# Kernel tuning notes

Hardware: AMD Instinct MI355X
Metric: run time of the kernel (lower is better)

## Reference

```python
import jax, jax.numpy as jnp
import numpy as np

BIT = 4
TOPK = 4
COEFF = 0.01
THD_POS = 2 ** (BIT - 1) - 1   # symmetric: +7
THD_NEG = -THD_POS             # symmetric: -7  -> 15 levels


def setup_inputs() -> dict:
    key = jax.random.key(0)
    k1, k2 = jax.random.split(key)
    weight = jax.random.normal(k1, (4096, 4096), dtype=jnp.float32)
    # positive per-channel quant step sizes, shape [out, 1]
    scale = jax.random.uniform(k2, (4096, 1), dtype=jnp.float32, minval=0.005, maxval=0.05)
    return {"weight": weight, "scale": scale}


def reference(weight, scale):
    # quantization level indices: [-7 .. 7], 15 levels
    q_range = jnp.arange(THD_NEG, THD_POS + 1, dtype=jnp.float32)      # [L]
    centers = scale * q_range                                          # [O, L] (per-channel)
    # broadcast squared distances: [O, I, L]
    d2 = (weight[:, :, None] - centers[:, None, :]) ** 2
    # torch.topk defaults to largest=True -> take k LARGEST squared distances
    vals, _ = jax.lax.top_k(d2, TOPK)                                  # [O, I, K], descending
    sm = jax.nn.softmax(vals, axis=-1)                                 # [O, I, K]
    loss = jnp.sum(vals * (1.0 - sm)) / (TOPK - 1)
    return loss * COEFF
```

## Files before the change

kernel.cpp:

```cpp
#include <hip/hip_runtime.h>


#define BLOCK 256
#define GRID  4096
#define S_F4  (GRID * BLOCK)
#define TILES 4

__device__ __forceinline__ float elem_loss(float wv, float s7, float s6,
                                           float s5, float s4) {
    const float a  = fabsf(wv);
    const float L0 = a + s7, L1 = a + s6, L2 = a + s5, L3 = a + s4;
    const float r0 = fabsf(s7 - a), r1 = fabsf(s6 - a);
    const float t0 = fmaxf(L0, r0);
    const float t1 = __builtin_amdgcn_fmed3f(r0, L0, L1);
    const float t2 = __builtin_amdgcn_fmed3f(r0, L1, L2);
    const float t3 = __builtin_amdgcn_fmed3f(r0, L2, L3);
    const float u0 = fmaxf(t0, r1);
    const float u1 = __builtin_amdgcn_fmed3f(r1, t0, t1);
    const float u2 = __builtin_amdgcn_fmed3f(r1, t1, t2);
    const float u3 = __builtin_amdgcn_fmed3f(r1, t2, t3);
    const float v0 = u0*u0, v1 = u1*u1, v2 = u2*u2, v3 = u3*u3;
    const float e1 = __expf(v1 - v0);
    const float e2 = __expf(v2 - v0);
    const float e3 = __expf(v3 - v0);
    const float Z   = 1.f + e1 + e2 + e3;
    const float dot = fmaf(v3, e3, fmaf(v2, e2, fmaf(v1, e1, v0)));
    return ((v0 + v1) + (v2 + v3)) - __fdividef(dot, Z);
}

__device__ __forceinline__ float quad_loss(float4 w4, float s) {
    const float s7 = 7.f*s, s6 = 6.f*s, s5 = 5.f*s, s4 = 4.f*s;
    return (elem_loss(w4.x, s7, s6, s5, s4) + elem_loss(w4.y, s7, s6, s5, s4))
         + (elem_loss(w4.z, s7, s6, s5, s4) + elem_loss(w4.w, s7, s6, s5, s4));
}

__global__ __launch_bounds__(BLOCK) void partial_kernel(
    const float4* __restrict__ w,
    const float* __restrict__ scale,
    float* __restrict__ partial)
{
    const int tid   = blockIdx.x * BLOCK + threadIdx.x;
    const int rbase = tid >> 10;

    float4 cw = w[tid];
    float  cs = scale[rbase];

    float acc = 0.f;
    #pragma unroll
    for (int m = 0; m < TILES; ++m) {
        float4 nw; float ns;
        if (m + 1 < TILES) {
            nw = w[tid + (m + 1) * S_F4];
            ns = scale[rbase + (m + 1) * 1024];
        }
        acc += quad_loss(cw, cs);
        if (m + 1 < TILES) { cw = nw; cs = ns; }
    }

    #pragma unroll
    for (int off = 32; off > 0; off >>= 1)
        acc += __shfl_down(acc, off, 64);
    __shared__ float lds[BLOCK / 64];
    const int lane = threadIdx.x & 63, wid = threadIdx.x >> 6;
    if (lane == 0) lds[wid] = acc;
    __syncthreads();
    if (threadIdx.x == 0) {
        float t = 0.f;
        #pragma unroll
        for (int q = 0; q < BLOCK / 64; ++q) t += lds[q];
        partial[blockIdx.x] = t;
    }
}

__global__ __launch_bounds__(1024) void reduce_kernel(
    const float* __restrict__ partial, float* __restrict__ out)
{
    float v = 0.f;
    #pragma unroll
    for (int k = 0; k < GRID / 1024; ++k)
        v += partial[threadIdx.x + k * 1024];
    #pragma unroll
    for (int off = 32; off > 0; off >>= 1)
        v += __shfl_down(v, off, 64);
    __shared__ float lds[16];
    const int lane = threadIdx.x & 63, wid = threadIdx.x >> 6;
    if (lane == 0) lds[wid] = v;
    __syncthreads();
    if (threadIdx.x == 0) {
        float t = 0.f;
        #pragma unroll
        for (int q = 0; q < 16; ++q) t += lds[q];
        out[0] = t * (0.01f / 3.0f);
    }
}

extern "C" void kernel_launch(void* const* d_in, const int* in_sizes, int n_in,
                              void* d_out, int out_size, void* d_ws, size_t ws_size,
                              hipStream_t stream) {
    const float4* weight4 = (const float4*)d_in[0];
    const float*  scale   = (const float*)d_in[1];
    float* out     = (float*)d_out;
    float* partial = (float*)d_ws;
    partial_kernel<<<GRID, BLOCK, 0, stream>>>(weight4, scale, partial);
    reduce_kernel<<<1, 1024, 0, stream>>>(partial, out);
}
```

Measured before the change: 104.0 us.

## Fold log2e into inputs, simplify top-k network, prefetch two tiles ahead

Scales weights and steps by sqrt(log2 e) so the softmax uses raw exp2 directly, and multiplies the final sum by ln2 to undo the scaling. Uses the fact that the largest distance is always |w|+7s to drop one max/med3 stage, and replaces the fast divide with rcp plus fma. Also deepens the load prefetch to two tiles ahead and adds an occupancy hint to launch bounds. The aim is fewer VALU instructions per element and better hiding of memory latency, at the cost of more registers and slightly different rounding.

```diff
diff --git a/kernel.cpp b/kernel.cpp
--- a/kernel.cpp
+++ b/kernel.cpp
@@ -5,36 +5,39 @@
 #define GRID  4096
 #define S_F4  (GRID * BLOCK)
 #define TILES 4
+#define C_SQRT_LOG2E 1.2011224087864498f
+#define LN2 0.69314718055994531f
 
 __device__ __forceinline__ float elem_loss(float wv, float s7, float s6,
                                            float s5, float s4) {
-    const float a  = fabsf(wv);
+    const float a  = fabsf(wv) * C_SQRT_LOG2E;
     const float L0 = a + s7, L1 = a + s6, L2 = a + s5, L3 = a + s4;
-    const float r0 = fabsf(s7 - a), r1 = fabsf(s6 - a);
-    const float t0 = fmaxf(L0, r0);
-    const float t1 = __builtin_amdgcn_fmed3f(r0, L0, L1);
+    const float r0 = fabsf(s7 - a);
+    const float r1 = fabsf(s6 - a);
+    const float t1 = fmaxf(r0, L1);
     const float t2 = __builtin_amdgcn_fmed3f(r0, L1, L2);
     const float t3 = __builtin_amdgcn_fmed3f(r0, L2, L3);
-    const float u0 = fmaxf(t0, r1);
-    const float u1 = __builtin_amdgcn_fmed3f(r1, t0, t1);
+    const float u1 = fmaxf(r1, t1);
     const float u2 = __builtin_amdgcn_fmed3f(r1, t1, t2);
     const float u3 = __builtin_amdgcn_fmed3f(r1, t2, t3);
-    const float v0 = u0*u0, v1 = u1*u1, v2 = u2*u2, v3 = u3*u3;
-    const float e1 = __expf(v1 - v0);
-    const float e2 = __expf(v2 - v0);
-    const float e3 = __expf(v3 - v0);
+    const float v0 = L0*L0, v1 = u1*u1, v2 = u2*u2, v3 = u3*u3;
+    const float e1 = __builtin_amdgcn_exp2f(v1 - v0);
+    const float e2 = __builtin_amdgcn_exp2f(v2 - v0);
+    const float e3 = __builtin_amdgcn_exp2f(v3 - v0);
     const float Z   = 1.f + e1 + e2 + e3;
     const float dot = fmaf(v3, e3, fmaf(v2, e2, fmaf(v1, e1, v0)));
-    return ((v0 + v1) + (v2 + v3)) - __fdividef(dot, Z);
+    const float sv  = (v0 + v1) + (v2 + v3);
+    return fmaf(-dot, __builtin_amdgcn_rcpf(Z), sv);
 }
 
 __device__ __forceinline__ float quad_loss(float4 w4, float s) {
-    const float s7 = 7.f*s, s6 = 6.f*s, s5 = 5.f*s, s4 = 4.f*s;
+    const float sq = s * C_SQRT_LOG2E;
+    const float s7 = 7.f*sq, s6 = 6.f*sq, s5 = 5.f*sq, s4 = 4.f*sq;
     return (elem_loss(w4.x, s7, s6, s5, s4) + elem_loss(w4.y, s7, s6, s5, s4))
          + (elem_loss(w4.z, s7, s6, s5, s4) + elem_loss(w4.w, s7, s6, s5, s4));
 }
 
-__global__ __launch_bounds__(BLOCK) void partial_kernel(
+__global__ __launch_bounds__(BLOCK, 8) void partial_kernel(
     const float4* __restrict__ w,
     const float* __restrict__ scale,
     float* __restrict__ partial)
@@ -42,19 +45,22 @@
     const int tid   = blockIdx.x * BLOCK + threadIdx.x;
     const int rbase = tid >> 10;
 
-    float4 cw = w[tid];
-    float  cs = scale[rbase];
+    float4 cw0 = w[tid];
+    float  cs0 = scale[rbase];
+    float4 cw1 = w[tid + S_F4];
+    float  cs1 = scale[rbase + 1024];
 
     float acc = 0.f;
     #pragma unroll
     for (int m = 0; m < TILES; ++m) {
         float4 nw; float ns;
-        if (m + 1 < TILES) {
-            nw = w[tid + (m + 1) * S_F4];
-            ns = scale[rbase + (m + 1) * 1024];
+        if (m + 2 < TILES) {
+            nw = w[tid + (m + 2) * S_F4];
+            ns = scale[rbase + (m + 2) * 1024];
         }
-        acc += quad_loss(cw, cs);
-        if (m + 1 < TILES) { cw = nw; cs = ns; }
+        acc += quad_loss(cw0, cs0);
+        cw0 = cw1; cs0 = cs1;
+        if (m + 2 < TILES) { cw1 = nw; cs1 = ns; }
     }
 
     #pragma unroll
@@ -90,7 +96,7 @@
         float t = 0.f;
         #pragma unroll
         for (int q = 0; q < 16; ++q) t += lds[q];
-        out[0] = t * (0.01f / 3.0f);
+        out[0] = t * (0.01f / 3.0f) * LN2;
     }
 }
 
```

Result: faster. 99.21 us (-4.6%).
